# Performance work log

Hardware: AMD Instinct MI355X
Metric: run time of the kernel (lower is better)

## Reference

```python
import jax, jax.numpy as jnp
import numpy as np

B, SEQ, D, N_LAYERS, HEADS, D_FF = 256, 43, 18, 6, 3, 2048
A_MAX, NB = 128, 7
EPS = 1e-6


def _norm(x, a, b):
    mu = x.mean(-1, keepdims=True)
    sd = jnp.std(x, axis=-1, ddof=1, keepdims=True)  # torch std is unbiased
    return a * (x - mu) / (sd + EPS) + b


def _attn(x, Wq, bq, Wk, bk, Wv, bv, Wo, bo, mask):
    b_, s, d = x.shape
    dk = d // HEADS
    def split_heads(W, bb):
        return (x @ W + bb).reshape(b_, s, HEADS, dk).transpose(0, 2, 1, 3)
    q, k, v = split_heads(Wq, bq), split_heads(Wk, bk), split_heads(Wv, bv)
    scores = jnp.einsum('bhqd,bhkd->bhqk', q, k) / jnp.sqrt(jnp.float32(dk))
    scores = jnp.where(mask[:, None, :, :] == 0, -1e9, scores)  # mask [B,1,S] -> [B,1,1,S]
    attn = jax.nn.softmax(scores, axis=-1)
    o = jnp.einsum('bhqk,bhkd->bhqd', attn, v).transpose(0, 2, 1, 3).reshape(b_, s, d)
    return o @ Wo + bo


def setup_inputs() -> dict:
    key = jax.random.key(0)
    ks = iter(jax.random.split(key, 40))
    g = lambda shape, s=0.05: jax.random.normal(next(ks), shape, dtype=jnp.float32) * s
    inp = {
        'src': jax.random.normal(next(ks), (B, SEQ, D), dtype=jnp.float32),
        'mask': jnp.ones((B, 1, SEQ), dtype=jnp.int32),
        'max_atoms': A_MAX,
        'enc_Wq': g((N_LAYERS, D, D)), 'enc_bq': g((N_LAYERS, D)),
        'enc_Wk': g((N_LAYERS, D, D)), 'enc_bk': g((N_LAYERS, D)),
        'enc_Wv': g((N_LAYERS, D, D)), 'enc_bv': g((N_LAYERS, D)),
        'enc_Wo': g((N_LAYERS, D, D)), 'enc_bo': g((N_LAYERS, D)),
        'enc_ln1_a': jnp.ones((N_LAYERS, D), jnp.float32), 'enc_ln1_b': jnp.zeros((N_LAYERS, D), jnp.float32),
        'enc_ln2_a': jnp.ones((N_LAYERS, D), jnp.float32), 'enc_ln2_b': jnp.zeros((N_LAYERS, D), jnp.float32),
        'enc_ffW1': g((N_LAYERS, D, D_FF)), 'enc_ffb1': g((N_LAYERS, D_FF)),
        'enc_ffW2': g((N_LAYERS, D_FF, D)), 'enc_ffb2': g((N_LAYERS, D)),
        'll2_W': g((D, A_MAX)), 'll2_b': g((A_MAX,)),
        'll_W': g((SEQ, A_MAX)), 'll_b': g((A_MAX,)),
        'fl_W': g((2 * A_MAX, NB)), 'fl_b': g((NB,)),
    }
    return inp


def reference(src, enc_Wq, enc_bq, enc_Wk, enc_bk, enc_Wv, enc_bv, enc_Wo, enc_bo,
              enc_ln1_a, enc_ln1_b, enc_ln2_a, enc_ln2_b,
              enc_ffW1, enc_ffb1, enc_ffW2, enc_ffb2,
              ll2_W, ll2_b, ll_W, ll_b, fl_W, fl_b, mask, max_atoms):
    # --- Encoder (dropout=0 at eval; no final norm, as in source) ---
    x = src
    for i in range(N_LAYERS):
        x2 = _norm(x, enc_ln1_a[i], enc_ln1_b[i])
        x = x + _attn(x2, enc_Wq[i], enc_bq[i], enc_Wk[i], enc_bk[i],
                      enc_Wv[i], enc_bv[i], enc_Wo[i], enc_bo[i], mask)
        x2 = _norm(x, enc_ln2_a[i], enc_ln2_b[i])
        x = x + (jax.nn.relu(x2 @ enc_ffW1[i] + enc_ffb1[i]) @ enc_ffW2[i] + enc_ffb2[i])
    # --- EdgeClassify2 ---
    red = x @ ll2_W + ll2_b            # [B, S, A]
    red = red.transpose(0, 2, 1)       # [B, A, S]
    R = red @ ll_W + ll_b              # [B, A, A]; repeat_e[:,i,i,:] == R[:,i,:]
    # final_e[b,i,j] = concat(R[b,i], R[b,j]); fl(concat) = R_i@W1 + R_j@W2 + b (exact)
    W1, W2 = fl_W[:max_atoms], fl_W[max_atoms:]
    P = R @ W1                          # [B, A, nb]
    Q = R @ W2                          # [B, A, nb]
    return P[:, :, None, :] + Q[:, None, :, :] + fl_b  # [B, A, A, nb]
```

## Files before the change

### kernel.cpp

```cpp
#include <hip/hip_runtime.h>
#include <math.h>

namespace {

constexpr int Sq = 43;
constexpr int Dm = 18;
constexpr int Dff = 2048;
constexpr int Am = 128;
constexpr int Nb = 7;
constexpr int NR = 11008;
constexpr int RSZ = NR * Dm;
constexpr int JC = 8;
constexpr int WROW = 20;
constexpr float EPSf = 1e-6f;

__device__ __forceinline__ void ln_qkv_write(
    int row, const float* y, int ly,
    const float* __restrict__ Wq, const float* __restrict__ bq,
    const float* __restrict__ Wk, const float* __restrict__ bk,
    const float* __restrict__ Wv, const float* __restrict__ bv,
    const float* __restrict__ ln1a, const float* __restrict__ ln1b,
    float* __restrict__ qb, float* __restrict__ kb, float* __restrict__ vb)
{
    float mu = 0.f;
    #pragma unroll
    for (int d = 0; d < Dm; d++) mu += y[d];
    mu *= (1.f / Dm);
    float var = 0.f;
    #pragma unroll
    for (int d = 0; d < Dm; d++) { float t = y[d] - mu; var += t * t; }
    var *= (1.f / (Dm - 1));
    float isd = 1.f / (sqrtf(var) + EPSf);
    float x2[Dm];
    #pragma unroll
    for (int d = 0; d < Dm; d++)
        x2[d] = ln1a[ly * Dm + d] * (y[d] - mu) * isd + ln1b[ly * Dm + d];
    const float* wq = Wq + ly * Dm * Dm;
    const float* wk = Wk + ly * Dm * Dm;
    const float* wv = Wv + ly * Dm * Dm;
    #pragma unroll 3
    for (int d = 0; d < Dm; d++) {
        float aq = bq[ly * Dm + d];
        float ak = bk[ly * Dm + d];
        float av = bv[ly * Dm + d];
        #pragma unroll
        for (int dd = 0; dd < Dm; dd++) {
            aq += x2[dd] * wq[dd * Dm + d];
            ak += x2[dd] * wk[dd * Dm + d];
            av += x2[dd] * wv[dd * Dm + d];
        }
        qb[(size_t)row * Dm + d] = aq;
        kb[(size_t)row * Dm + d] = ak;
        vb[(size_t)row * Dm + d] = av;
    }
}

__global__ __launch_bounds__(256) void k_wprep(
    const float* __restrict__ W1g, const float* __restrict__ b1g,
    const float* __restrict__ W2g,
    float* __restrict__ W1P, float* __restrict__ W2P)
{
    const int idx = blockIdx.x * 256 + threadIdx.x;
    const int l = idx / Dff;
    const int j = idx - l * Dff;
    float* o1 = W1P + (size_t)idx * WROW;
    float* o2 = W2P + (size_t)idx * WROW;
    #pragma unroll
    for (int d = 0; d < Dm; d++)
        o1[d] = W1g[(size_t)l * Dm * Dff + (size_t)d * Dff + j];
    o1[18] = b1g[l * Dff + j];
    o1[19] = 0.f;
    #pragma unroll
    for (int d = 0; d < Dm; d++)
        o2[d] = W2g[((size_t)l * Dff + j) * Dm + d];
    o2[18] = 0.f;
    o2[19] = 0.f;
    if (idx < WROW) {
        W1P[(size_t)6 * Dff * WROW + idx] = 0.f;
        W2P[(size_t)6 * Dff * WROW + idx] = 0.f;
    }
}

__global__ __launch_bounds__(64) void k_init(
    const float* __restrict__ src, float* __restrict__ xg,
    const float* __restrict__ Wq, const float* __restrict__ bq,
    const float* __restrict__ Wk, const float* __restrict__ bk,
    const float* __restrict__ Wv, const float* __restrict__ bv,
    const float* __restrict__ ln1a, const float* __restrict__ ln1b,
    float* __restrict__ qb, float* __restrict__ kb, float* __restrict__ vb,
    const float* __restrict__ llW, const float* __restrict__ llb,
    const float* __restrict__ flW, const float* __restrict__ flb,
    const float* __restrict__ ll2b,
    float* __restrict__ Mw, float* __restrict__ PS1, float* __restrict__ QS2)
{
    __shared__ float M[602];
    __shared__ float cc2[14];
    __shared__ float SS[14];
    const int tid = threadIdx.x;

    if (blockIdx.x == 172) {
        for (int m = tid; m < 602; m += 64) {
            int half = m / 301, rem = m - half * 301;
            int s = rem / 7, n = rem - 7 * s;
            float a = 0.f;
            for (int jj = 0; jj < Am; jj++)
                a += llW[s * Am + jj] * flW[(half * Am + jj) * Nb + n];
            M[m] = a;
        }
        if (tid < 14) {
            int half = tid / 7, n = tid - 7 * (tid / 7);
            float a = 0.f;
            for (int jj = 0; jj < Am; jj++)
                a += llb[jj] * flW[(half * Am + jj) * Nb + n];
            cc2[tid] = a;
        }
        __syncthreads();
        if (tid < 14) {
            int half = tid / 7, n = tid - 7 * (tid / 7);
            float s2 = 0.f;
            for (int s = 0; s < Sq; s++) s2 += M[half * 301 + s * 7 + n];
            SS[tid] = s2;
        }
        __syncthreads();
        for (int m = tid; m < 602; m += 64) Mw[m] = M[m];
        for (int m = tid; m < 896; m += 64) {
            int i = m / 7, n = m - 7 * i;
            PS1[m] = cc2[n] + ll2b[i] * SS[n];
            QS2[m] = cc2[7 + n] + ll2b[i] * SS[7 + n] + flb[n];
        }
        return;
    }

    int row = blockIdx.x * 64 + tid;
    float y[Dm];
    #pragma unroll
    for (int d = 0; d < Dm; d++) {
        y[d] = src[(size_t)row * Dm + d];
        xg[(size_t)row * Dm + d] = y[d];
    }
    ln_qkv_write(row, y, 0, Wq, bq, Wk, bk, Wv, bv, ln1a, ln1b, qb, kb, vb);
}

__global__ __launch_bounds__(64) void k_attn(
    int layer,
    const float* __restrict__ qb, const float* __restrict__ kb,
    const float* __restrict__ vb, const int* __restrict__ maskg,
    const float* __restrict__ xg, float* __restrict__ xn,
    float* __restrict__ x2g,
    const float* __restrict__ Wo, const float* __restrict__ bo,
    const float* __restrict__ ln2a, const float* __restrict__ ln2b,
    const float* __restrict__ b2g)
{
    __shared__ __align__(16) float ks[Sq * 20];
    __shared__ __align__(16) float vs[Sq * 20];
    __shared__ int ms[Sq];

    const int b = blockIdx.x;
    const int tid = threadIdx.x;
    const float scale = 0.40824829046386296f;

    for (int e = tid; e < Sq * Dm; e += 64) {
        int r = e / 18, d = e - 18 * r;
        ks[r * 20 + d] = kb[(size_t)b * (Sq * Dm) + e];
        vs[r * 20 + d] = vb[(size_t)b * (Sq * Dm) + e];
    }
    if (tid < Sq) ms[tid] = maskg[b * Sq + tid];
    __syncthreads();

    if (tid >= Sq) return;
    const int row = b * Sq + tid;

    float qv[Dm];
    #pragma unroll
    for (int d = 0; d < Dm; d++) qv[d] = qb[(size_t)row * Dm + d];

    float o[Dm];
    #pragma unroll
    for (int h = 0; h < 3; h++) {
        float sum = 0.f;
        float o6[6];
        #pragma unroll
        for (int d = 0; d < 6; d++) o6[d] = 0.f;
        const float q0 = qv[h * 6], q1 = qv[h * 6 + 1], q2 = qv[h * 6 + 2];
        const float q3 = qv[h * 6 + 3], q4 = qv[h * 6 + 4], q5 = qv[h * 6 + 5];
        for (int j = 0; j < Sq; j++) {
            const float* kr = ks + j * 20 + h * 6;
            const float2 k0 = *(const float2*)(kr);
            const float2 k1 = *(const float2*)(kr + 2);
            const float2 k2 = *(const float2*)(kr + 4);
            float t = q0 * k0.x + q1 * k0.y + q2 * k1.x +
                      q3 * k1.y + q4 * k2.x + q5 * k2.y;
            t *= scale;
            if (ms[j] == 0) t = -1e9f;
            float e = __expf(t);
            sum += e;
            const float* vr = vs + j * 20 + h * 6;
            const float2 v0 = *(const float2*)(vr);
            const float2 v1 = *(const float2*)(vr + 2);
            const float2 v2 = *(const float2*)(vr + 4);
            o6[0] += e * v0.x; o6[1] += e * v0.y; o6[2] += e * v1.x;
            o6[3] += e * v1.y; o6[4] += e * v2.x; o6[5] += e * v2.y;
        }
        float inv = 1.f / sum;
        #pragma unroll
        for (int d = 0; d < 6; d++) o[h * 6 + d] = o6[d] * inv;
    }

    const float* wo = Wo + layer * Dm * Dm;
    float y[Dm];
    #pragma unroll 3
    for (int d = 0; d < Dm; d++) {
        float t = bo[layer * Dm + d];
        #pragma unroll
        for (int dd = 0; dd < Dm; dd++) t += o[dd] * wo[dd * Dm + d];
        y[d] = xg[(size_t)row * Dm + d] + t;
    }
    #pragma unroll
    for (int d = 0; d < Dm; d++)
        xn[(size_t)row * Dm + d] = y[d] + b2g[layer * Dm + d];
    float mu = 0.f;
    #pragma unroll
    for (int d = 0; d < Dm; d++) mu += y[d];
    mu *= (1.f / Dm);
    float var = 0.f;
    #pragma unroll
    for (int d = 0; d < Dm; d++) { float t = y[d] - mu; var += t * t; }
    var *= (1.f / (Dm - 1));
    float isd = 1.f / (sqrtf(var) + EPSf);
    #pragma unroll
    for (int d = 0; d < Dm; d++)
        x2g[(size_t)row * Dm + d] =
            ln2a[layer * Dm + d] * (y[d] - mu) * isd + ln2b[layer * Dm + d];
}

__global__ __launch_bounds__(256, 3) void k_ffn(
    int layer, const float* __restrict__ x2g,
    const float* __restrict__ W1P, const float* __restrict__ W2P,
    float* __restrict__ P)
{
    __shared__ float Ls[4 * 64 * Dm];

    const int tid  = threadIdx.x;
    const int lane = tid & 63;
    const int wv   = __builtin_amdgcn_readfirstlane(tid >> 6);
    const int rg   = blockIdx.x >> 3;
    const int q    = blockIdx.x & 7;
    const int row  = rg * 64 + lane;
    const int j0   = q * 256 + wv * 64;

    const float4* w1p = (const float4*)(W1P + ((size_t)layer * Dff + j0) * WROW);
    const float4* w2p = (const float4*)(W2P + ((size_t)layer * Dff + j0) * WROW);

    float x[Dm];
    #pragma unroll
    for (int k = 0; k < 9; k++) {
        float2 t = *(const float2*)(x2g + (size_t)row * Dm + 2 * k);
        x[2 * k] = t.x; x[2 * k + 1] = t.y;
    }
    float acc[Dm];
    #pragma unroll
    for (int d = 0; d < Dm; d++) acc[d] = 0.f;

    float4 a0 = w1p[0], a1 = w1p[1], a2 = w1p[2], a3 = w1p[3], a4 = w1p[4];
    float4 c0 = w2p[0], c1 = w2p[1], c2 = w2p[2], c3 = w2p[3], c4 = w2p[4];

    for (int jj = 0; jj < 64; jj++) {
        const float4* n1 = w1p + (jj + 1) * 5;
        const float4* n2 = w2p + (jj + 1) * 5;
        const float4 na0 = n1[0], na1 = n1[1], na2 = n1[2], na3 = n1[3], na4 = n1[4];
        const float4 nc0 = n2[0], nc1 = n2[1], nc2 = n2[2], nc3 = n2[3], nc4 = n2[4];

        float h = a4.z
            + x[0]  * a0.x + x[1]  * a0.y + x[2]  * a0.z + x[3]  * a0.w
            + x[4]  * a1.x + x[5]  * a1.y + x[6]  * a1.z + x[7]  * a1.w
            + x[8]  * a2.x + x[9]  * a2.y + x[10] * a2.z + x[11] * a2.w
            + x[12] * a3.x + x[13] * a3.y + x[14] * a3.z + x[15] * a3.w
            + x[16] * a4.x + x[17] * a4.y;
        h = fmaxf(h, 0.f);
        acc[0]  += h * c0.x;  acc[1]  += h * c0.y;
        acc[2]  += h * c0.z;  acc[3]  += h * c0.w;
        acc[4]  += h * c1.x;  acc[5]  += h * c1.y;
        acc[6]  += h * c1.z;  acc[7]  += h * c1.w;
        acc[8]  += h * c2.x;  acc[9]  += h * c2.y;
        acc[10] += h * c2.z;  acc[11] += h * c2.w;
        acc[12] += h * c3.x;  acc[13] += h * c3.y;
        acc[14] += h * c3.z;  acc[15] += h * c3.w;
        acc[16] += h * c4.x;  acc[17] += h * c4.y;

        a0 = na0; a1 = na1; a2 = na2; a3 = na3; a4 = na4;
        c0 = nc0; c1 = nc1; c2 = nc2; c3 = nc3; c4 = nc4;
    }

    #pragma unroll
    for (int d = 0; d < Dm; d++)
        Ls[(wv * 64 + lane) * Dm + d] = acc[d];
    __syncthreads();
    for (int e = tid; e < 1152; e += 256) {
        float s = Ls[e] + Ls[1152 + e] + Ls[2304 + e] + Ls[3456 + e];
        P[(size_t)q * RSZ + (size_t)rg * 1152 + e] = s;
    }
}

__global__ __launch_bounds__(64) void k_post(
    int layer, float* __restrict__ xn, const float* __restrict__ P,
    int do_tail,
    const float* __restrict__ Wq, const float* __restrict__ bq,
    const float* __restrict__ Wk, const float* __restrict__ bk,
    const float* __restrict__ Wv, const float* __restrict__ bv,
    const float* __restrict__ ln1a, const float* __restrict__ ln1b,
    float* __restrict__ qb, float* __restrict__ kb, float* __restrict__ vb)
{
    const int row = blockIdx.x * 64 + threadIdx.x;
    float y[Dm];
    #pragma unroll
    for (int d = 0; d < Dm; d++) {
        size_t o = (size_t)row * Dm + d;
        float t = xn[o];
        #pragma unroll
        for (int c = 0; c < JC; c++) t += P[(size_t)c * RSZ + o];
        y[d] = t;
        xn[o] = t;
    }
    if (do_tail)
        ln_qkv_write(row, y, layer + 1, Wq, bq, Wk, bk, Wv, bv,
                     ln1a, ln1b, qb, kb, vb);
}

__global__ __launch_bounds__(256) void k_out(
    const float* __restrict__ xg, const float* __restrict__ ll2W,
    const float* __restrict__ Mw, const float* __restrict__ PS1,
    const float* __restrict__ QS2, float* __restrict__ out)
{
    __shared__ float xb[Sq * Dm];
    __shared__ float M[602];
    __shared__ float T[2][Dm][Nb];
    __shared__ float Pc[32 * Nb];
    __shared__ float QBs[Am * Nb];

    const int b = blockIdx.y, chunk = blockIdx.x, tid = threadIdx.x;

    for (int e = tid; e < Sq * Dm; e += 256) xb[e] = xg[(size_t)b * (Sq * Dm) + e];
    for (int m = tid; m < 602; m += 256) M[m] = Mw[m];
    __syncthreads();

    for (int m = tid; m < 252; m += 256) {
        int half = m / 126, rem = m - half * 126;
        int d = rem / 7, n = rem - 7 * d;
        float a = 0.f;
        for (int s = 0; s < Sq; s++)
            a += xb[s * Dm + d] * M[half * 301 + s * 7 + n];
        T[half][d][n] = a;
    }
    __syncthreads();

    for (int m = tid; m < 224; m += 256) {
        int il = m / 7, n = m - 7 * il;
        int i = chunk * 32 + il;
        float a = PS1[i * 7 + n];
        #pragma unroll
        for (int d = 0; d < Dm; d++) a += T[0][d][n] * ll2W[d * Am + i];
        Pc[m] = a;
    }
    for (int e = tid; e < 896; e += 256) {
        int jj = e / 7, n = e - 7 * jj;
        float a = QS2[e];
        #pragma unroll
        for (int d = 0; d < Dm; d++) a += T[1][d][n] * ll2W[d * Am + jj];
        QBs[e] = a;
    }
    __syncthreads();

    if (tid < 224) {
        const int e = 4 * tid;
        const float q0 = QBs[e], q1 = QBs[e + 1], q2 = QBs[e + 2], q3 = QBs[e + 3];
        const int n0 = e % 7, n1 = (e + 1) % 7, n2 = (e + 2) % 7, n3 = (e + 3) % 7;
        const size_t base = (size_t)b * (Am * Am * Nb)
                          + (size_t)chunk * 32 * 896 + e;
        for (int il = 0; il < 32; il++) {
            const float* pc = Pc + il * 7;
            float4 v;
            v.x = pc[n0] + q0; v.y = pc[n1] + q1;
            v.z = pc[n2] + q2; v.w = pc[n3] + q3;
            *(float4*)(out + base + (size_t)il * 896) = v;
        }
    }
}

}

extern "C" void kernel_launch(void* const* d_in, const int* in_sizes, int n_in,
                              void* d_out, int out_size, void* d_ws, size_t ws_size,
                              hipStream_t stream)
{
    (void)in_sizes; (void)n_in; (void)out_size; (void)ws_size;

    const float* src  = (const float*)d_in[0];
    const int*   mask = (const int*)  d_in[1];
    const float* Wq   = (const float*)d_in[3];
    const float* bq   = (const float*)d_in[4];
    const float* Wk   = (const float*)d_in[5];
    const float* bk   = (const float*)d_in[6];
    const float* Wv   = (const float*)d_in[7];
    const float* bv   = (const float*)d_in[8];
    const float* Wo   = (const float*)d_in[9];
    const float* bo   = (const float*)d_in[10];
    const float* ln1a = (const float*)d_in[11];
    const float* ln1b = (const float*)d_in[12];
    const float* ln2a = (const float*)d_in[13];
    const float* ln2b = (const float*)d_in[14];
    const float* fW1  = (const float*)d_in[15];
    const float* fb1  = (const float*)d_in[16];
    const float* fW2  = (const float*)d_in[17];
    const float* fb2  = (const float*)d_in[18];
    const float* ll2W = (const float*)d_in[19];
    const float* ll2b = (const float*)d_in[20];
    const float* llW  = (const float*)d_in[21];
    const float* llb  = (const float*)d_in[22];
    const float* flW  = (const float*)d_in[23];
    const float* flb  = (const float*)d_in[24];
    float* out = (float*)d_out;

    const size_t WPSZ = (size_t)6 * Dff * WROW + WROW;

    float* ws  = (float*)d_ws;
    float* xA  = ws;
    float* xB  = ws + 1 * (size_t)RSZ;
    float* x2g = ws + 2 * (size_t)RSZ;
    float* qb  = ws + 3 * (size_t)RSZ;
    float* kb  = ws + 4 * (size_t)RSZ;
    float* vb  = ws + 5 * (size_t)RSZ;
    float* P   = ws + 6 * (size_t)RSZ;
    float* W1P = ws + (6 + JC) * (size_t)RSZ;
    float* W2P = W1P + WPSZ;
    float* Mw  = W2P + WPSZ;
    float* PS1 = Mw + 604;
    float* QS2 = PS1 + 896;

    k_wprep<<<48, 256, 0, stream>>>(fW1, fb1, fW2, W1P, W2P);
    k_init<<<173, 64, 0, stream>>>(src, xA, Wq, bq, Wk, bk, Wv, bv,
                                   ln1a, ln1b, qb, kb, vb,
                                   llW, llb, flW, flb, ll2b, Mw, PS1, QS2);
    for (int i = 0; i < 6; i++) {
        const float* Xi = (i % 2 == 0) ? xA : xB;
        float*       Xn = (i % 2 == 0) ? xB : xA;
        k_attn<<<256, 64, 0, stream>>>(i, qb, kb, vb, mask, Xi, Xn, x2g,
                                       Wo, bo, ln2a, ln2b, fb2);
        k_ffn<<<1376, 256, 0, stream>>>(i, x2g, W1P, W2P, P);
        k_post<<<172, 64, 0, stream>>>(i, Xn, P, (i < 5) ? 1 : 0,
                                       Wq, bq, Wk, bk, Wv, bv,
                                       ln1a, ln1b, qb, kb, vb);
    }
    k_out<<<dim3(4, 256), 256, 0, stream>>>(xA, ll2W, Mw, PS1, QS2, out);
}
```

Measured before the change: 603.1 us.

## Fuse residual reduction, LN1 and QKV projection into attention kernel; fold setup kernels

Removes the k_post, k_init and k_wprep launches. Each attention block now sums the FFN partial outputs into the residual, applies LN1, computes Q/K/V directly into shared memory, then runs attention. Weight repacking and the output-constant precomputation move into extra blocks of the first attention launch, and k_out does the final partial-sum reduction itself. This cuts 8 kernel launches and the global round trip of q/k/v buffers. In exchange, the attention launch does more serial per-row work before its barrier.

```diff
diff --git a/kernel.cpp b/kernel.cpp
--- a/kernel.cpp
+++ b/kernel.cpp
@@ -14,91 +14,59 @@
 constexpr int WROW = 20;
 constexpr float EPSf = 1e-6f;
 
-__device__ __forceinline__ void ln_qkv_write(
-    int row, const float* y, int ly,
+__global__ __launch_bounds__(64) void k_attn(
+    int layer,
+    const float* __restrict__ Xi, float* __restrict__ Xn,
+    float* __restrict__ x2g, const float* __restrict__ Pp,
+    const int* __restrict__ maskg,
     const float* __restrict__ Wq, const float* __restrict__ bq,
     const float* __restrict__ Wk, const float* __restrict__ bk,
     const float* __restrict__ Wv, const float* __restrict__ bv,
     const float* __restrict__ ln1a, const float* __restrict__ ln1b,
-    float* __restrict__ qb, float* __restrict__ kb, float* __restrict__ vb)
-{
-    float mu = 0.f;
-    #pragma unroll
-    for (int d = 0; d < Dm; d++) mu += y[d];
-    mu *= (1.f / Dm);
-    float var = 0.f;
-    #pragma unroll
-    for (int d = 0; d < Dm; d++) { float t = y[d] - mu; var += t * t; }
-    var *= (1.f / (Dm - 1));
-    float isd = 1.f / (sqrtf(var) + EPSf);
-    float x2[Dm];
-    #pragma unroll
-    for (int d = 0; d < Dm; d++)
-        x2[d] = ln1a[ly * Dm + d] * (y[d] - mu) * isd + ln1b[ly * Dm + d];
-    const float* wq = Wq + ly * Dm * Dm;
-    const float* wk = Wk + ly * Dm * Dm;
-    const float* wv = Wv + ly * Dm * Dm;
-    #pragma unroll 3
-    for (int d = 0; d < Dm; d++) {
-        float aq = bq[ly * Dm + d];
-        float ak = bk[ly * Dm + d];
-        float av = bv[ly * Dm + d];
-        #pragma unroll
-        for (int dd = 0; dd < Dm; dd++) {
-            aq += x2[dd] * wq[dd * Dm + d];
-            ak += x2[dd] * wk[dd * Dm + d];
-            av += x2[dd] * wv[dd * Dm + d];
-        }
-        qb[(size_t)row * Dm + d] = aq;
-        kb[(size_t)row * Dm + d] = ak;
-        vb[(size_t)row * Dm + d] = av;
-    }
-}
-
-__global__ __launch_bounds__(256) void k_wprep(
-    const float* __restrict__ W1g, const float* __restrict__ b1g,
-    const float* __restrict__ W2g,
-    float* __restrict__ W1P, float* __restrict__ W2P)
-{
-    const int idx = blockIdx.x * 256 + threadIdx.x;
-    const int l = idx / Dff;
-    const int j = idx - l * Dff;
-    float* o1 = W1P + (size_t)idx * WROW;
-    float* o2 = W2P + (size_t)idx * WROW;
-    #pragma unroll
-    for (int d = 0; d < Dm; d++)
-        o1[d] = W1g[(size_t)l * Dm * Dff + (size_t)d * Dff + j];
-    o1[18] = b1g[l * Dff + j];
-    o1[19] = 0.f;
-    #pragma unroll
-    for (int d = 0; d < Dm; d++)
-        o2[d] = W2g[((size_t)l * Dff + j) * Dm + d];
-    o2[18] = 0.f;
-    o2[19] = 0.f;
-    if (idx < WROW) {
-        W1P[(size_t)6 * Dff * WROW + idx] = 0.f;
-        W2P[(size_t)6 * Dff * WROW + idx] = 0.f;
-    }
-}
-
-__global__ __launch_bounds__(64) void k_init(
-    const float* __restrict__ src, float* __restrict__ xg,
-    const float* __restrict__ Wq, const float* __restrict__ bq,
-    const float* __restrict__ Wk, const float* __restrict__ bk,
-    const float* __restrict__ Wv, const float* __restrict__ bv,
-    const float* __restrict__ ln1a, const float* __restrict__ ln1b,
-    float* __restrict__ qb, float* __restrict__ kb, float* __restrict__ vb,
+    const float* __restrict__ Wo, const float* __restrict__ bo,
+    const float* __restrict__ ln2a, const float* __restrict__ ln2b,
+    const float* __restrict__ b2g,
+    const float* __restrict__ fW1g, const float* __restrict__ fb1g,
+    const float* __restrict__ fW2g,
+    float* __restrict__ W1P, float* __restrict__ W2P,
     const float* __restrict__ llW, const float* __restrict__ llb,
     const float* __restrict__ flW, const float* __restrict__ flb,
     const float* __restrict__ ll2b,
     float* __restrict__ Mw, float* __restrict__ PS1, float* __restrict__ QS2)
 {
+    __shared__ __align__(16) float ks[Sq * 20];
+    __shared__ __align__(16) float vs[Sq * 20];
+    __shared__ int ms[Sq];
     __shared__ float M[602];
     __shared__ float cc2[14];
     __shared__ float SS[14];
+
     const int tid = threadIdx.x;
-
-    if (blockIdx.x == 172) {
+    const int b = blockIdx.x;
+
+    if (b >= 256) {
+        if (b < 448) {
+            const int idx = (b - 256) * 64 + tid;
+            const int l = idx / Dff;
+            const int j = idx - l * Dff;
+            float* o1 = W1P + (size_t)idx * WROW;
+            float* o2 = W2P + (size_t)idx * WROW;
+            #pragma unroll
+            for (int d = 0; d < Dm; d++)
+                o1[d] = fW1g[(size_t)l * Dm * Dff + (size_t)d * Dff + j];
+            o1[18] = fb1g[l * Dff + j];
+            o1[19] = 0.f;
+            #pragma unroll
+            for (int d = 0; d < Dm; d++)
+                o2[d] = fW2g[((size_t)l * Dff + j) * Dm + d];
+            o2[18] = 0.f;
+            o2[19] = 0.f;
+            if (idx < WROW) {
+                W1P[(size_t)6 * Dff * WROW + idx] = 0.f;
+                W2P[(size_t)6 * Dff * WROW + idx] = 0.f;
+            }
+            return;
+        }
         for (int m = tid; m < 602; m += 64) {
             int half = m / 301, rem = m - half * 301;
             int s = rem / 7, n = rem - 7 * s;
@@ -131,48 +99,58 @@
         return;
     }
 
-    int row = blockIdx.x * 64 + tid;
+    const float scale = 0.40824829046386296f;
+
+    if (tid < Sq) ms[tid] = maskg[b * Sq + tid];
+
     float y[Dm];
-    #pragma unroll
-    for (int d = 0; d < Dm; d++) {
-        y[d] = src[(size_t)row * Dm + d];
-        xg[(size_t)row * Dm + d] = y[d];
-    }
-    ln_qkv_write(row, y, 0, Wq, bq, Wk, bk, Wv, bv, ln1a, ln1b, qb, kb, vb);
-}
-
-__global__ __launch_bounds__(64) void k_attn(
-    int layer,
-    const float* __restrict__ qb, const float* __restrict__ kb,
-    const float* __restrict__ vb, const int* __restrict__ maskg,
-    const float* __restrict__ xg, float* __restrict__ xn,
-    float* __restrict__ x2g,
-    const float* __restrict__ Wo, const float* __restrict__ bo,
-    const float* __restrict__ ln2a, const float* __restrict__ ln2b,
-    const float* __restrict__ b2g)
-{
-    __shared__ __align__(16) float ks[Sq * 20];
-    __shared__ __align__(16) float vs[Sq * 20];
-    __shared__ int ms[Sq];
-
-    const int b = blockIdx.x;
-    const int tid = threadIdx.x;
-    const float scale = 0.40824829046386296f;
-
-    for (int e = tid; e < Sq * Dm; e += 64) {
-        int r = e / 18, d = e - 18 * r;
-        ks[r * 20 + d] = kb[(size_t)b * (Sq * Dm) + e];
-        vs[r * 20 + d] = vb[(size_t)b * (Sq * Dm) + e];
-    }
-    if (tid < Sq) ms[tid] = maskg[b * Sq + tid];
+    float qv[Dm];
+    if (tid < Sq) {
+        const size_t ro = (size_t)(b * Sq + tid) * Dm;
+        #pragma unroll
+        for (int d = 0; d < Dm; d++) {
+            float t = Xi[ro + d];
+            if (layer > 0) {
+                #pragma unroll
+                for (int c = 0; c < JC; c++) t += Pp[(size_t)c * RSZ + ro + d];
+            }
+            y[d] = t;
+        }
+        float mu = 0.f;
+        #pragma unroll
+        for (int d = 0; d < Dm; d++) mu += y[d];
+        mu *= (1.f / Dm);
+        float var = 0.f;
+        #pragma unroll
+        for (int d = 0; d < Dm; d++) { float t = y[d] - mu; var += t * t; }
+        var *= (1.f / (Dm - 1));
+        float isd = 1.f / (sqrtf(var) + EPSf);
+        float x2[Dm];
+        #pragma unroll
+        for (int d = 0; d < Dm; d++)
+            x2[d] = ln1a[layer * Dm + d] * (y[d] - mu) * isd
+                  + ln1b[layer * Dm + d];
+        const float* wqp = Wq + layer * Dm * Dm;
+        const float* wkp = Wk + layer * Dm * Dm;
+        const float* wvp = Wv + layer * Dm * Dm;
+        #pragma unroll 3
+        for (int d = 0; d < Dm; d++) {
+            float aq = bq[layer * Dm + d];
+            float ak = bk[layer * Dm + d];
+            float av = bv[layer * Dm + d];
+            #pragma unroll
+            for (int dd = 0; dd < Dm; dd++) {
+                aq += x2[dd] * wqp[dd * Dm + d];
+                ak += x2[dd] * wkp[dd * Dm + d];
+                av += x2[dd] * wvp[dd * Dm + d];
+            }
+            qv[d] = aq;
+            ks[tid * 20 + d] = ak;
+            vs[tid * 20 + d] = av;
+        }
+    }
     __syncthreads();
-
     if (tid >= Sq) return;
-    const int row = b * Sq + tid;
-
-    float qv[Dm];
-    #pragma unroll
-    for (int d = 0; d < Dm; d++) qv[d] = qb[(size_t)row * Dm + d];
 
     float o[Dm];
     #pragma unroll
@@ -207,30 +185,31 @@
     }
 
     const float* wo = Wo + layer * Dm * Dm;
-    float y[Dm];
+    float yo[Dm];
     #pragma unroll 3
     for (int d = 0; d < Dm; d++) {
         float t = bo[layer * Dm + d];
         #pragma unroll
         for (int dd = 0; dd < Dm; dd++) t += o[dd] * wo[dd * Dm + d];
-        y[d] = xg[(size_t)row * Dm + d] + t;
-    }
+        yo[d] = y[d] + t;
+    }
+    const size_t ro = (size_t)(b * Sq + tid) * Dm;
     #pragma unroll
     for (int d = 0; d < Dm; d++)
-        xn[(size_t)row * Dm + d] = y[d] + b2g[layer * Dm + d];
+        Xn[ro + d] = yo[d] + b2g[layer * Dm + d];
     float mu = 0.f;
     #pragma unroll
-    for (int d = 0; d < Dm; d++) mu += y[d];
+    for (int d = 0; d < Dm; d++) mu += yo[d];
     mu *= (1.f / Dm);
     float var = 0.f;
     #pragma unroll
-    for (int d = 0; d < Dm; d++) { float t = y[d] - mu; var += t * t; }
+    for (int d = 0; d < Dm; d++) { float t = yo[d] - mu; var += t * t; }
     var *= (1.f / (Dm - 1));
     float isd = 1.f / (sqrtf(var) + EPSf);
     #pragma unroll
     for (int d = 0; d < Dm; d++)
-        x2g[(size_t)row * Dm + d] =
-            ln2a[layer * Dm + d] * (y[d] - mu) * isd + ln2b[layer * Dm + d];
+        x2g[ro + d] =
+            ln2a[layer * Dm + d] * (yo[d] - mu) * isd + ln2b[layer * Dm + d];
 }
 
 __global__ __launch_bounds__(256, 3) void k_ffn(
@@ -301,33 +280,9 @@
     }
 }
 
-__global__ __launch_bounds__(64) void k_post(
-    int layer, float* __restrict__ xn, const float* __restrict__ P,
-    int do_tail,
-    const float* __restrict__ Wq, const float* __restrict__ bq,
-    const float* __restrict__ Wk, const float* __restrict__ bk,
-    const float* __restrict__ Wv, const float* __restrict__ bv,
-    const float* __restrict__ ln1a, const float* __restrict__ ln1b,
-    float* __restrict__ qb, float* __restrict__ kb, float* __restrict__ vb)
-{
-    const int row = blockIdx.x * 64 + threadIdx.x;
-    float y[Dm];
-    #pragma unroll
-    for (int d = 0; d < Dm; d++) {
-        size_t o = (size_t)row * Dm + d;
-        float t = xn[o];
-        #pragma unroll
-        for (int c = 0; c < JC; c++) t += P[(size_t)c * RSZ + o];
-        y[d] = t;
-        xn[o] = t;
-    }
-    if (do_tail)
-        ln_qkv_write(row, y, layer + 1, Wq, bq, Wk, bk, Wv, bv,
-                     ln1a, ln1b, qb, kb, vb);
-}
-
 __global__ __launch_bounds__(256) void k_out(
-    const float* __restrict__ xg, const float* __restrict__ ll2W,
+    const float* __restrict__ xg, const float* __restrict__ Pp,
+    const float* __restrict__ ll2W,
     const float* __restrict__ Mw, const float* __restrict__ PS1,
     const float* __restrict__ QS2, float* __restrict__ out)
 {
@@ -339,7 +294,13 @@
 
     const int b = blockIdx.y, chunk = blockIdx.x, tid = threadIdx.x;
 
-    for (int e = tid; e < Sq * Dm; e += 256) xb[e] = xg[(size_t)b * (Sq * Dm) + e];
+    for (int e = tid; e < Sq * Dm; e += 256) {
+        const size_t o = (size_t)b * (Sq * Dm) + e;
+        float t = xg[o];
+        #pragma unroll
+        for (int c = 0; c < JC; c++) t += Pp[(size_t)c * RSZ + o];
+        xb[e] = t;
+    }
     for (int m = tid; m < 602; m += 256) M[m] = Mw[m];
     __syncthreads();
 
@@ -426,29 +387,24 @@
     float* xA  = ws;
     float* xB  = ws + 1 * (size_t)RSZ;
     float* x2g = ws + 2 * (size_t)RSZ;
-    float* qb  = ws + 3 * (size_t)RSZ;
-    float* kb  = ws + 4 * (size_t)RSZ;
-    float* vb  = ws + 5 * (size_t)RSZ;
-    float* P   = ws + 6 * (size_t)RSZ;
-    float* W1P = ws + (6 + JC) * (size_t)RSZ;
+    float* P   = ws + 3 * (size_t)RSZ;
+    float* W1P = ws + (3 + JC) * (size_t)RSZ;
     float* W2P = W1P + WPSZ;
     float* Mw  = W2P + WPSZ;
     float* PS1 = Mw + 604;
     float* QS2 = PS1 + 896;
 
-    k_wprep<<<48, 256, 0, stream>>>(fW1, fb1, fW2, W1P, W2P);
-    k_init<<<173, 64, 0, stream>>>(src, xA, Wq, bq, Wk, bk, Wv, bv,
-                                   ln1a, ln1b, qb, kb, vb,
-                                   llW, llb, flW, flb, ll2b, Mw, PS1, QS2);
     for (int i = 0; i < 6; i++) {
-        const float* Xi = (i % 2 == 0) ? xA : xB;
+        const float* Xi = (i == 0) ? src : ((i % 2 == 1) ? xB : xA);
         float*       Xn = (i % 2 == 0) ? xB : xA;
-        k_attn<<<256, 64, 0, stream>>>(i, qb, kb, vb, mask, Xi, Xn, x2g,
-                                       Wo, bo, ln2a, ln2b, fb2);
+        const int nblk = (i == 0) ? 449 : 256;
+        k_attn<<<nblk, 64, 0, stream>>>(i, Xi, Xn, x2g, P, mask,
+                                        Wq, bq, Wk, bk, Wv, bv,
+                                        ln1a, ln1b, Wo, bo, ln2a, ln2b, fb2,
+                                        fW1, fb1, fW2, W1P, W2P,
+                                        llW, llb, flW, flb, ll2b,
+                                        Mw, PS1, QS2);
         k_ffn<<<1376, 256, 0, stream>>>(i, x2g, W1P, W2P, P);
-        k_post<<<172, 64, 0, stream>>>(i, Xn, P, (i < 5) ? 1 : 0,
-                                       Wq, bq, Wk, bk, Wv, bv,
-                                       ln1a, ln1b, qb, kb, vb);
-    }
-    k_out<<<dim3(4, 256), 256, 0, stream>>>(xA, ll2W, Mw, PS1, QS2, out);
+    }
+    k_out<<<dim3(4, 256), 256, 0, stream>>>(xA, P, ll2W, Mw, PS1, QS2, out);
 }
```

Result: faster. 568.9 us (-5.7%).
